# Kernel tuning notes

Hardware: AMD Instinct MI355X
Metric: run time of the kernel (lower is better)

## Reference

```python
import jax, jax.numpy as jnp
import numpy as np

# Sampled 2-layer GraphSAGE sizes (ogbn-products-like, fanouts [25, 10], batch 4096)
N0, N1, N2 = 1_000_000, 40_960, 4_096   # source nodes per hop / targets
E1, E2 = 1_024_000, 40_960              # edges per hop
IN_C, HID, OUT = 100, 256, 47


def setup_inputs() -> dict:
    key = jax.random.key(0)
    ks = jax.random.split(key, 10)
    x = jax.random.normal(ks[0], (N0, IN_C), jnp.float32)
    src1 = jax.random.randint(ks[1], (E1,), 0, N0, dtype=jnp.int64)
    dst1 = jax.random.randint(ks[2], (E1,), 0, N1, dtype=jnp.int64)
    src2 = jax.random.randint(ks[3], (E2,), 0, N1, dtype=jnp.int64)
    dst2 = jax.random.randint(ks[4], (E2,), 0, N2, dtype=jnp.int64)
    s1 = 1.0 / np.sqrt(IN_C)
    s2 = 1.0 / np.sqrt(HID)
    W1l = jax.random.uniform(ks[5], (IN_C, HID), jnp.float32, -s1, s1)
    W1r = jax.random.uniform(ks[6], (IN_C, HID), jnp.float32, -s1, s1)
    b1l = jnp.zeros((HID,), jnp.float32)
    W2l = jax.random.uniform(ks[7], (HID, OUT), jnp.float32, -s2, s2)
    W2r = jax.random.uniform(ks[8], (HID, OUT), jnp.float32, -s2, s2)
    b2l = jnp.zeros((OUT,), jnp.float32)
    return {"x": x, "W1l": W1l, "b1l": b1l, "W1r": W1r,
            "W2l": W2l, "b2l": b2l, "W2r": W2r,
            "src1": src1, "dst1": dst1, "src2": src2, "dst2": dst2}


def _sage_conv(x_src, x_dst, src, dst, Wl, bl, Wr, num_dst):
    # PyG SAGEConv (aggr='mean'): lin_l(mean_j x_j) + lin_r(x_target)
    msg = x_src[src]                                            # [E, C] gather
    agg = jax.ops.segment_sum(msg, dst, num_segments=num_dst)   # [num_dst, C]
    cnt = jax.ops.segment_sum(jnp.ones((src.shape[0], 1), x_src.dtype), dst,
                              num_segments=num_dst)
    agg = agg / jnp.maximum(cnt, 1.0)                           # mean (0 for isolated)
    return agg @ Wl + bl + x_dst @ Wr


def reference(x, W1l, b1l, W1r, W2l, b2l, W2r, src1, dst1, src2, dst2):
    # layer 1: bipartite (N0 -> N1)
    h = _sage_conv(x, x[:N1], src1, dst1, W1l, b1l, W1r, N1)
    h = jax.nn.relu(h)  # dropout is identity in eval mode
    # layer 2: bipartite (N1 -> N2)
    out = _sage_conv(h, h[:N2], src2, dst2, W2l, b2l, W2r, N2)
    return jax.nn.log_softmax(out, axis=-1)
```

## Files before the change

kernel.cpp:

```cpp
#include <hip/hip_runtime.h>
#include <math.h>

#define N0 1000000
#define N1 40960
#define N2 4096
#define E1 1024000
#define E2 40960
#define IN_C 100
#define HID 256
#define OUT_C 47
#define S1 128
#define S2 64

__global__ __launch_bounds__(256) void build_kernel(
    const int* __restrict__ src1, const int* __restrict__ dst1,
    const int* __restrict__ src2, const int* __restrict__ dst2,
    int* __restrict__ deg1, int* __restrict__ ell1,
    int* __restrict__ deg2, int* __restrict__ ell2) {
    int gid = blockIdx.x * 256 + threadIdx.x;
    if (gid < E1) {
        int d = dst1[gid];
        int slot = atomicAdd(&deg1[d], 1);
        if (slot < S1) ell1[d * S1 + slot] = src1[gid];
    } else if (gid < E1 + E2) {
        int e = gid - E1;
        int d = dst2[e];
        int slot = atomicAdd(&deg2[d], 1);
        if (slot < S2) ell2[d * S2 + slot] = src2[e];
    }
}

__global__ __launch_bounds__(256) void agg1_kernel(
    const float* __restrict__ x, const int* __restrict__ ell1,
    const int* __restrict__ deg1, float* __restrict__ aggm1) {
    int d = (blockIdx.x << 2) + (threadIdx.x >> 6);
    int lane = threadIdx.x & 63;
    int nd = deg1[d];
    int n = (nd < S1) ? nd : S1;
    const int* rp = ell1 + d * S1;
    int c1 = 64 + lane;
    int c1m = (c1 < IN_C) ? c1 : 0;
    float a0 = 0.f, a1 = 0.f, b0 = 0.f, b1 = 0.f;
    int e = 0;
    for (; e + 3 < n; e += 4) {
        int s0 = rp[e], s1 = rp[e + 1], s2 = rp[e + 2], s3 = rp[e + 3];
        const float* p0 = x + s0 * IN_C;
        const float* p1 = x + s1 * IN_C;
        const float* p2 = x + s2 * IN_C;
        const float* p3 = x + s3 * IN_C;
        float v0 = p0[lane], v1 = p1[lane], v2 = p2[lane], v3 = p3[lane];
        float w0 = p0[c1m], w1 = p1[c1m], w2 = p2[c1m], w3 = p3[c1m];
        a0 += v0 + v1; b0 += v2 + v3;
        a1 += w0 + w1; b1 += w2 + w3;
    }
    for (; e < n; ++e) {
        int s = rp[e];
        const float* p = x + s * IN_C;
        a0 += p[lane];
        a1 += p[c1m];
    }
    a0 += b0; a1 += b1;
    float inv = 1.0f / (float)(nd > 0 ? nd : 1);
    aggm1[d * IN_C + lane] = a0 * inv;
    if (c1 < IN_C) aggm1[d * IN_C + c1] = a1 * inv;
}

__global__ __launch_bounds__(256) void gemm1_kernel(
    const float* __restrict__ aggm1, const float* __restrict__ x,
    const float* __restrict__ W1l, const float* __restrict__ b1l,
    const float* __restrict__ W1r, float* __restrict__ h) {
    __shared__ float axs[32][2 * IN_C];
    int tid = threadIdx.x;
    int i0 = blockIdx.x * 32;
    for (int idx = tid; idx < 32 * IN_C; idx += 256) {
        int r = idx / IN_C;
        int k = idx - r * IN_C;
        int row = i0 + r;
        axs[r][2 * k]     = aggm1[row * IN_C + k];
        axs[r][2 * k + 1] = x[row * IN_C + k];
    }
    __syncthreads();

    int jq = tid & 63;
    int rgrp = tid >> 6;
    int j4 = jq * 4;
    const float4* wl = (const float4*)(W1l + j4);
    const float4* wr = (const float4*)(W1r + j4);
    const float4* ax4 = (const float4*)(&axs[rgrp * 8][0]);

    float acc[8][4];
    #pragma unroll
    for (int r = 0; r < 8; ++r)
        #pragma unroll
        for (int c = 0; c < 4; ++c) acc[r][c] = 0.f;

    for (int k = 0; k < IN_C; k += 2) {
        float4 wl0 = wl[k * 64];
        float4 wr0 = wr[k * 64];
        float4 wl1 = wl[(k + 1) * 64];
        float4 wr1 = wr[(k + 1) * 64];
        int kh = k >> 1;
        #pragma unroll
        for (int r = 0; r < 8; ++r) {
            float4 v = ax4[r * 50 + kh];
            acc[r][0] += v.x * wl0.x + v.y * wr0.x + v.z * wl1.x + v.w * wr1.x;
            acc[r][1] += v.x * wl0.y + v.y * wr0.y + v.z * wl1.y + v.w * wr1.y;
            acc[r][2] += v.x * wl0.z + v.y * wr0.z + v.z * wl1.z + v.w * wr1.z;
            acc[r][3] += v.x * wl0.w + v.y * wr0.w + v.z * wl1.w + v.w * wr1.w;
        }
    }

    float4 b = *(const float4*)(b1l + j4);
    #pragma unroll
    for (int r = 0; r < 8; ++r) {
        int row = i0 + rgrp * 8 + r;
        float4 o;
        o.x = fmaxf(acc[r][0] + b.x, 0.f);
        o.y = fmaxf(acc[r][1] + b.y, 0.f);
        o.z = fmaxf(acc[r][2] + b.z, 0.f);
        o.w = fmaxf(acc[r][3] + b.w, 0.f);
        *(float4*)(h + row * HID + j4) = o;
    }
}

__global__ __launch_bounds__(256) void l2_fused_kernel(
    const float* __restrict__ h, const int* __restrict__ ell2,
    const int* __restrict__ deg2,
    const float* __restrict__ W2l, const float* __restrict__ b2l,
    const float* __restrict__ W2r, float* __restrict__ out) {
    __shared__ float sa[4][HID];
    __shared__ float sh_[4][HID];
    int w = threadIdx.x >> 6;
    int lane = threadIdx.x & 63;
    int row = (blockIdx.x << 2) + w;

    int nd = deg2[row];
    int n = (nd < S2) ? nd : S2;
    const int* rp = ell2 + row * S2;
    float4 acc4 = {0.f, 0.f, 0.f, 0.f};
    int e = 0;
    for (; e + 1 < n; e += 2) {
        int s0 = rp[e], s1 = rp[e + 1];
        float4 v0 = ((const float4*)(h + s0 * HID))[lane];
        float4 v1 = ((const float4*)(h + s1 * HID))[lane];
        acc4.x += v0.x + v1.x; acc4.y += v0.y + v1.y;
        acc4.z += v0.z + v1.z; acc4.w += v0.w + v1.w;
    }
    if (e < n) {
        int s0 = rp[e];
        float4 v0 = ((const float4*)(h + s0 * HID))[lane];
        acc4.x += v0.x; acc4.y += v0.y; acc4.z += v0.z; acc4.w += v0.w;
    }
    float inv = 1.0f / (float)(nd > 0 ? nd : 1);
    float4 am = {acc4.x * inv, acc4.y * inv, acc4.z * inv, acc4.w * inv};
    ((float4*)&sa[w][0])[lane] = am;
    ((float4*)&sh_[w][0])[lane] = ((const float4*)(h + row * HID))[lane];
    __syncthreads();

    int j = lane;
    int jj = (j < OUT_C) ? j : (OUT_C - 1);
    float acc = 0.f;
    for (int k = 0; k < HID; k += 4) {
        float4 av = *(const float4*)&sa[w][k];
        float4 hv = *(const float4*)&sh_[w][k];
        acc += av.x * W2l[(k + 0) * OUT_C + jj] + hv.x * W2r[(k + 0) * OUT_C + jj];
        acc += av.y * W2l[(k + 1) * OUT_C + jj] + hv.y * W2r[(k + 1) * OUT_C + jj];
        acc += av.z * W2l[(k + 2) * OUT_C + jj] + hv.z * W2r[(k + 2) * OUT_C + jj];
        acc += av.w * W2l[(k + 3) * OUT_C + jj] + hv.w * W2r[(k + 3) * OUT_C + jj];
    }
    float v = acc + b2l[jj];
    float vm = (j < OUT_C) ? v : -__builtin_huge_valf();
    #pragma unroll
    for (int s = 32; s > 0; s >>= 1) vm = fmaxf(vm, __shfl_xor(vm, s));
    float ex = (j < OUT_C) ? __expf(v - vm) : 0.f;
    #pragma unroll
    for (int s = 32; s > 0; s >>= 1) ex += __shfl_xor(ex, s);
    if (j < OUT_C) out[row * OUT_C + j] = v - vm - __logf(ex);
}

extern "C" void kernel_launch(void* const* d_in, const int* in_sizes, int n_in,
                              void* d_out, int out_size, void* d_ws, size_t ws_size,
                              hipStream_t stream) {
    const float* x   = (const float*)d_in[0];
    const float* W1l = (const float*)d_in[1];
    const float* b1l = (const float*)d_in[2];
    const float* W1r = (const float*)d_in[3];
    const float* W2l = (const float*)d_in[4];
    const float* b2l = (const float*)d_in[5];
    const float* W2r = (const float*)d_in[6];
    const int* src1  = (const int*)d_in[7];
    const int* dst1  = (const int*)d_in[8];
    const int* src2  = (const int*)d_in[9];
    const int* dst2  = (const int*)d_in[10];
    float* out = (float*)d_out;

    char* ws = (char*)d_ws;
    size_t off = 0;
    auto alloc = [&](size_t bytes) {
        off = (off + 255) & ~(size_t)255;
        void* p = ws + off;
        off += bytes;
        return p;
    };

    int* deg1 = (int*)alloc(N1 * sizeof(int));
    int* deg2 = (int*)alloc(N2 * sizeof(int));
    int* ell1 = (int*)alloc((size_t)N1 * S1 * sizeof(int));
    int* ell2 = (int*)alloc((size_t)N2 * S2 * sizeof(int));
    float* aggm1 = (float*)alloc((size_t)N1 * IN_C * sizeof(float));
    float* h     = (float*)alloc((size_t)N1 * HID * sizeof(float));

    hipMemsetAsync(deg1, 0, (N1 + N2) * sizeof(int), stream);

    build_kernel<<<(E1 + E2) / 256, 256, 0, stream>>>(src1, dst1, src2, dst2,
                                                      deg1, ell1, deg2, ell2);
    agg1_kernel<<<N1 / 4, 256, 0, stream>>>(x, ell1, deg1, aggm1);
    gemm1_kernel<<<N1 / 32, 256, 0, stream>>>(aggm1, x, W1l, b1l, W1r, h);
    l2_fused_kernel<<<N2 / 4, 256, 0, stream>>>(h, ell2, deg2, W2l, b2l, W2r, out);
}
```

Baseline: 706.4 us.

## Fuse layer-1 neighbor aggregation into GEMM kernel and vectorize edge build

Layer-1 mean aggregation is moved into the GEMM kernel. Each wave gathers 8 rows into shared memory before the matmul, which removes the aggm1 intermediate buffer and one kernel launch. The build kernel now processes two edges per thread using int2 loads. The tradeoff is fewer, longer-running blocks and less parallelism for the latency-bound gather.

```diff
diff --git a/kernel.cpp b/kernel.cpp
--- a/kernel.cpp
+++ b/kernel.cpp
@@ -18,71 +18,78 @@
     int* __restrict__ deg1, int* __restrict__ ell1,
     int* __restrict__ deg2, int* __restrict__ ell2) {
     int gid = blockIdx.x * 256 + threadIdx.x;
-    if (gid < E1) {
-        int d = dst1[gid];
-        int slot = atomicAdd(&deg1[d], 1);
-        if (slot < S1) ell1[d * S1 + slot] = src1[gid];
-    } else if (gid < E1 + E2) {
-        int e = gid - E1;
-        int d = dst2[e];
-        int slot = atomicAdd(&deg2[d], 1);
-        if (slot < S2) ell2[d * S2 + slot] = src2[e];
-    }
-}
-
-__global__ __launch_bounds__(256) void agg1_kernel(
+    if (gid < E1 / 2) {
+        int2 s = ((const int2*)src1)[gid];
+        int2 d = ((const int2*)dst1)[gid];
+        int slot0 = atomicAdd(&deg1[d.x], 1);
+        if (slot0 < S1) ell1[d.x * S1 + slot0] = s.x;
+        int slot1 = atomicAdd(&deg1[d.y], 1);
+        if (slot1 < S1) ell1[d.y * S1 + slot1] = s.y;
+    } else {
+        int p = gid - E1 / 2;
+        int2 s = ((const int2*)src2)[p];
+        int2 d = ((const int2*)dst2)[p];
+        int slot0 = atomicAdd(&deg2[d.x], 1);
+        if (slot0 < S2) ell2[d.x * S2 + slot0] = s.x;
+        int slot1 = atomicAdd(&deg2[d.y], 1);
+        if (slot1 < S2) ell2[d.y * S2 + slot1] = s.y;
+    }
+}
+
+__global__ __launch_bounds__(256) void fused1_kernel(
     const float* __restrict__ x, const int* __restrict__ ell1,
-    const int* __restrict__ deg1, float* __restrict__ aggm1) {
-    int d = (blockIdx.x << 2) + (threadIdx.x >> 6);
-    int lane = threadIdx.x & 63;
-    int nd = deg1[d];
-    int n = (nd < S1) ? nd : S1;
-    const int* rp = ell1 + d * S1;
-    int c1 = 64 + lane;
-    int c1m = (c1 < IN_C) ? c1 : 0;
-    float a0 = 0.f, a1 = 0.f, b0 = 0.f, b1 = 0.f;
-    int e = 0;
-    for (; e + 3 < n; e += 4) {
-        int s0 = rp[e], s1 = rp[e + 1], s2 = rp[e + 2], s3 = rp[e + 3];
-        const float* p0 = x + s0 * IN_C;
-        const float* p1 = x + s1 * IN_C;
-        const float* p2 = x + s2 * IN_C;
-        const float* p3 = x + s3 * IN_C;
-        float v0 = p0[lane], v1 = p1[lane], v2 = p2[lane], v3 = p3[lane];
-        float w0 = p0[c1m], w1 = p1[c1m], w2 = p2[c1m], w3 = p3[c1m];
-        a0 += v0 + v1; b0 += v2 + v3;
-        a1 += w0 + w1; b1 += w2 + w3;
-    }
-    for (; e < n; ++e) {
-        int s = rp[e];
-        const float* p = x + s * IN_C;
-        a0 += p[lane];
-        a1 += p[c1m];
-    }
-    a0 += b0; a1 += b1;
-    float inv = 1.0f / (float)(nd > 0 ? nd : 1);
-    aggm1[d * IN_C + lane] = a0 * inv;
-    if (c1 < IN_C) aggm1[d * IN_C + c1] = a1 * inv;
-}
-
-__global__ __launch_bounds__(256) void gemm1_kernel(
-    const float* __restrict__ aggm1, const float* __restrict__ x,
+    const int* __restrict__ deg1,
     const float* __restrict__ W1l, const float* __restrict__ b1l,
     const float* __restrict__ W1r, float* __restrict__ h) {
     __shared__ float axs[32][2 * IN_C];
     int tid = threadIdx.x;
+    int lane = tid & 63;
+    int w = tid >> 6;
     int i0 = blockIdx.x * 32;
+
     for (int idx = tid; idx < 32 * IN_C; idx += 256) {
         int r = idx / IN_C;
         int k = idx - r * IN_C;
+        axs[r][2 * k + 1] = x[(i0 + r) * IN_C + k];
+    }
+
+    int c1 = 64 + lane;
+    int c1m = (c1 < IN_C) ? c1 : 0;
+    #pragma unroll 1
+    for (int rr = 0; rr < 8; ++rr) {
+        int r = w * 8 + rr;
         int row = i0 + r;
-        axs[r][2 * k]     = aggm1[row * IN_C + k];
-        axs[r][2 * k + 1] = x[row * IN_C + k];
+        int nd = deg1[row];
+        int n = (nd < S1) ? nd : S1;
+        const int* rp = ell1 + row * S1;
+        float a0 = 0.f, a1 = 0.f, b0 = 0.f, b1 = 0.f;
+        int e = 0;
+        for (; e + 3 < n; e += 4) {
+            int s0 = rp[e], s1 = rp[e + 1], s2 = rp[e + 2], s3 = rp[e + 3];
+            const float* p0 = x + s0 * IN_C;
+            const float* p1 = x + s1 * IN_C;
+            const float* p2 = x + s2 * IN_C;
+            const float* p3 = x + s3 * IN_C;
+            float v0 = p0[lane], v1 = p1[lane], v2 = p2[lane], v3 = p3[lane];
+            float w0 = p0[c1m], w1 = p1[c1m], w2 = p2[c1m], w3 = p3[c1m];
+            a0 += v0 + v1; b0 += v2 + v3;
+            a1 += w0 + w1; b1 += w2 + w3;
+        }
+        for (; e < n; ++e) {
+            int s = rp[e];
+            const float* p = x + s * IN_C;
+            a0 += p[lane];
+            a1 += p[c1m];
+        }
+        a0 += b0; a1 += b1;
+        float inv = 1.0f / (float)(nd > 0 ? nd : 1);
+        axs[r][2 * lane] = a0 * inv;
+        if (c1 < IN_C) axs[r][2 * c1] = a1 * inv;
     }
     __syncthreads();
 
-    int jq = tid & 63;
-    int rgrp = tid >> 6;
+    int jq = lane;
+    int rgrp = w;
     int j4 = jq * 4;
     const float4* wl = (const float4*)(W1l + j4);
     const float4* wr = (const float4*)(W1r + j4);
@@ -207,14 +214,12 @@
     int* deg2 = (int*)alloc(N2 * sizeof(int));
     int* ell1 = (int*)alloc((size_t)N1 * S1 * sizeof(int));
     int* ell2 = (int*)alloc((size_t)N2 * S2 * sizeof(int));
-    float* aggm1 = (float*)alloc((size_t)N1 * IN_C * sizeof(float));
-    float* h     = (float*)alloc((size_t)N1 * HID * sizeof(float));
+    float* h  = (float*)alloc((size_t)N1 * HID * sizeof(float));
 
     hipMemsetAsync(deg1, 0, (N1 + N2) * sizeof(int), stream);
 
-    build_kernel<<<(E1 + E2) / 256, 256, 0, stream>>>(src1, dst1, src2, dst2,
-                                                      deg1, ell1, deg2, ell2);
-    agg1_kernel<<<N1 / 4, 256, 0, stream>>>(x, ell1, deg1, aggm1);
-    gemm1_kernel<<<N1 / 32, 256, 0, stream>>>(aggm1, x, W1l, b1l, W1r, h);
+    build_kernel<<<(E1 / 2 + E2 / 2) / 256, 256, 0, stream>>>(
+        src1, dst1, src2, dst2, deg1, ell1, deg2, ell2);
+    fused1_kernel<<<N1 / 32, 256, 0, stream>>>(x, ell1, deg1, W1l, b1l, W1r, h);
     l2_fused_kernel<<<N2 / 4, 256, 0, stream>>>(h, ell2, deg2, W2l, b2l, W2r, out);
 }
```

Measured after the change: 751.0 us. 1.06x slower.
